# Kernel optimization log

Measured on AMD Instinct MI355X. Metric: run time of the kernel, lower is better.

## Reference

```python
import jax, jax.numpy as jnp
import numpy as np

TEMPERATURE = 0.1


def setup_inputs() -> dict:
    key = jax.random.key(0)
    k1, k2 = jax.random.split(key)
    pred = jax.random.normal(k1, (4, 64, 32), dtype=jnp.float32)
    target = jax.random.normal(k2, (4, 64, 32), dtype=jnp.float32)
    return {"pred": pred, "target": target}


def reference(pred, target):
    # All inputs are finite and no mask is given, so valid_both is all-True and
    # the torch boolean flatten pred[valid_both] is exactly a reshape(-1).
    p = pred.reshape(-1)
    t = target.reshape(-1)
    n = p.shape[0]  # 8192
    # diff[i, j] = x[j] - x[i]; product is symmetric so orientation is irrelevant.
    pd = p[None, :] - p[:, None]           # [n, n]
    td = t[None, :] - t[:, None]           # [n, n]
    agreement = jnp.tanh(pd * td / TEMPERATURE)
    # mean over strict upper triangle (i < j): mask-and-sum, divide by pair count.
    upper = jnp.triu(jnp.ones((n, n), dtype=agreement.dtype), k=1)
    n_pairs = jnp.asarray(n * (n - 1) // 2, dtype=agreement.dtype)
    tau = jnp.sum(agreement * upper) / n_pairs
    return tau
```

## Files before the change

### kernel.cpp

```cpp
#include <hip/hip_runtime.h>


#define NTOT 8192
#define TPB  512
#define KPT  (NTOT / TPB)
#define JBLK 8
#define NBLK (NTOT / JBLK)

__global__ __launch_bounds__(TPB) void ktau_partial(const float* __restrict__ pred,
                                                    const float* __restrict__ targ,
                                                    double* __restrict__ partial) {
    const float C = 28.853900817779268f;
    const int tid = threadIdx.x;
    const int j0  = blockIdx.x * JBLK;

    float pj[JBLK], tj[JBLK];
#pragma unroll
    for (int jj = 0; jj < JBLK; ++jj) {
        pj[jj] = pred[j0 + jj];
        tj[jj] = targ[j0 + jj] * C;
    }

    float pi[KPT], ti[KPT];
#pragma unroll
    for (int k = 0; k < KPT; ++k) {
        const int i = tid + k * TPB;
        pi[k] = pred[i];
        ti[k] = targ[i] * C;
    }

    float acc[JBLK];
#pragma unroll
    for (int jj = 0; jj < JBLK; ++jj) acc[jj] = 0.0f;

#pragma unroll 2
    for (int k = 0; k < KPT; ++k) {
#pragma unroll
        for (int jj = 0; jj < JBLK; ++jj) {
            const float x = (pi[k] - pj[jj]) * (ti[k] - tj[jj]);
            const float e = __builtin_amdgcn_exp2f(x);
            const float r = __builtin_amdgcn_rcpf(e + 1.0f);
            acc[jj] = __builtin_fmaf(-2.0f, r, acc[jj]);
        }
    }

    float fsum = 0.0f;
#pragma unroll
    for (int jj = 0; jj < JBLK; ++jj) fsum += acc[jj];

    double dacc = (double)fsum;
#pragma unroll
    for (int off = 32; off > 0; off >>= 1)
        dacc += __shfl_down(dacc, off, 64);

    __shared__ double red[TPB / 64];
    const int wave = tid >> 6;
    if ((tid & 63) == 0) red[wave] = dacc;
    __syncthreads();
    if (tid == 0) {
        double s = 0.0;
#pragma unroll
        for (int w = 0; w < TPB / 64; ++w) s += red[w];
        partial[blockIdx.x] = s + (double)(TPB * KPT * JBLK);
    }
}

__global__ __launch_bounds__(256) void ktau_final(const double* __restrict__ partial,
                                                  float* __restrict__ out) {
    const int tid = threadIdx.x;
    double s = partial[tid] + partial[tid + 256] + partial[tid + 512] + partial[tid + 768];
#pragma unroll
    for (int off = 32; off > 0; off >>= 1)
        s += __shfl_down(s, off, 64);
    __shared__ double red[4];
    if ((tid & 63) == 0) red[tid >> 6] = s;
    __syncthreads();
    if (tid == 0) {
        const double t = red[0] + red[1] + red[2] + red[3];
        out[0] = (float)(t / ((double)NTOT * (double)(NTOT - 1)));
    }
}

extern "C" void kernel_launch(void* const* d_in, const int* in_sizes, int n_in,
                              void* d_out, int out_size, void* d_ws, size_t ws_size,
                              hipStream_t stream) {
    const float* pred = (const float*)d_in[0];
    const float* targ = (const float*)d_in[1];
    float* out = (float*)d_out;
    double* partial = (double*)d_ws;

    ktau_partial<<<NBLK, TPB, 0, stream>>>(pred, targ, partial);
    ktau_final<<<1, 256, 0, stream>>>(partial, out);
}
```

Baseline: 71.44 us.

## Exploit pair symmetry by computing only upper-triangular tile pairs

Replaces the full n×n sweep with a triangular grid of 128×128 tile pairs, decoding the tile row and column from the block index with a sqrt. Diagonal tiles are halved and the normaliser becomes the pair count, so roughly half of the exp/rcp evaluations are skipped. The j values are staged in shared memory and read as float4, at the cost of a per-block index decode, a barrier, and more partials in the final reduction.

```diff
diff --git a/kernel.cpp b/kernel.cpp
--- a/kernel.cpp
+++ b/kernel.cpp
@@ -2,42 +2,58 @@
 
 
 #define NTOT 8192
-#define TPB  512
-#define KPT  (NTOT / TPB)
-#define JBLK 8
-#define NBLK (NTOT / JBLK)
+#define TILE 128
+#define NT   (NTOT / TILE)
+#define NBLK (NT * (NT + 1) / 2)
+#define TPB  256
 
-__global__ __launch_bounds__(TPB) void ktau_partial(const float* __restrict__ pred,
-                                                    const float* __restrict__ targ,
-                                                    double* __restrict__ partial) {
+__device__ __forceinline__ int rowoff(int a) {
+    return a * NT - (a * (a - 1)) / 2;
+}
+
+__global__ __launch_bounds__(TPB) void ktau_tri(const float* __restrict__ pred,
+                                                const float* __restrict__ targ,
+                                                double* __restrict__ partial) {
     const float C = 28.853900817779268f;
     const int tid = threadIdx.x;
-    const int j0  = blockIdx.x * JBLK;
+    const int bid = blockIdx.x;
 
-    float pj[JBLK], tj[JBLK];
-#pragma unroll
-    for (int jj = 0; jj < JBLK; ++jj) {
-        pj[jj] = pred[j0 + jj];
-        tj[jj] = targ[j0 + jj] * C;
+    int a = (int)((2.0 * NT + 1.0 -
+                   sqrt((2.0 * NT + 1.0) * (2.0 * NT + 1.0) - 8.0 * (double)bid)) * 0.5);
+    while (rowoff(a + 1) <= bid) ++a;
+    while (a > 0 && rowoff(a) > bid) --a;
+    const int b = a + (bid - rowoff(a));
+
+    __shared__ float sjp[TILE];
+    __shared__ float sjt[TILE];
+    if (tid < TILE) {
+        sjp[tid] = pred[b * TILE + tid];
+        sjt[tid] = targ[b * TILE + tid] * C;
     }
 
-    float pi[KPT], ti[KPT];
+    const int il = tid & (TILE - 1);
+    const int jh = tid >> 7;
+    const float pi = pred[a * TILE + il];
+    const float ti = targ[a * TILE + il] * C;
+    __syncthreads();
+
+    float acc[8];
 #pragma unroll
-    for (int k = 0; k < KPT; ++k) {
-        const int i = tid + k * TPB;
-        pi[k] = pred[i];
-        ti[k] = targ[i] * C;
-    }
+    for (int jj = 0; jj < 8; ++jj) acc[jj] = 0.0f;
 
-    float acc[JBLK];
+    const float4* sp4 = (const float4*)sjp;
+    const float4* st4 = (const float4*)sjt;
+
 #pragma unroll
-    for (int jj = 0; jj < JBLK; ++jj) acc[jj] = 0.0f;
-
-#pragma unroll 2
-    for (int k = 0; k < KPT; ++k) {
+    for (int jc = 0; jc < 8; ++jc) {
+        const int q = jh * 16 + jc * 2;
+        const float4 pj0 = sp4[q],     pj1 = sp4[q + 1];
+        const float4 tj0 = st4[q],     tj1 = st4[q + 1];
+        const float pj[8] = {pj0.x, pj0.y, pj0.z, pj0.w, pj1.x, pj1.y, pj1.z, pj1.w};
+        const float tj[8] = {tj0.x, tj0.y, tj0.z, tj0.w, tj1.x, tj1.y, tj1.z, tj1.w};
 #pragma unroll
-        for (int jj = 0; jj < JBLK; ++jj) {
-            const float x = (pi[k] - pj[jj]) * (ti[k] - tj[jj]);
+        for (int jj = 0; jj < 8; ++jj) {
+            const float x = (pi - pj[jj]) * (ti - tj[jj]);
             const float e = __builtin_amdgcn_exp2f(x);
             const float r = __builtin_amdgcn_rcpf(e + 1.0f);
             acc[jj] = __builtin_fmaf(-2.0f, r, acc[jj]);
@@ -46,7 +62,7 @@
 
     float fsum = 0.0f;
 #pragma unroll
-    for (int jj = 0; jj < JBLK; ++jj) fsum += acc[jj];
+    for (int jj = 0; jj < 8; ++jj) fsum += acc[jj];
 
     double dacc = (double)fsum;
 #pragma unroll
@@ -54,21 +70,22 @@
         dacc += __shfl_down(dacc, off, 64);
 
     __shared__ double red[TPB / 64];
-    const int wave = tid >> 6;
-    if ((tid & 63) == 0) red[wave] = dacc;
+    if ((tid & 63) == 0) red[tid >> 6] = dacc;
     __syncthreads();
     if (tid == 0) {
         double s = 0.0;
 #pragma unroll
         for (int w = 0; w < TPB / 64; ++w) s += red[w];
-        partial[blockIdx.x] = s + (double)(TPB * KPT * JBLK);
+        s += (double)(TPB * 64);
+        partial[bid] = (a == b) ? 0.5 * s : s;
     }
 }
 
 __global__ __launch_bounds__(256) void ktau_final(const double* __restrict__ partial,
                                                   float* __restrict__ out) {
     const int tid = threadIdx.x;
-    double s = partial[tid] + partial[tid + 256] + partial[tid + 512] + partial[tid + 768];
+    double s = 0.0;
+    for (int t = tid; t < NBLK; t += 256) s += partial[t];
 #pragma unroll
     for (int off = 32; off > 0; off >>= 1)
         s += __shfl_down(s, off, 64);
@@ -76,8 +93,8 @@
     if ((tid & 63) == 0) red[tid >> 6] = s;
     __syncthreads();
     if (tid == 0) {
-        const double t = red[0] + red[1] + red[2] + red[3];
-        out[0] = (float)(t / ((double)NTOT * (double)(NTOT - 1)));
+        const double n_pairs = (double)NTOT * (double)(NTOT - 1) * 0.5;
+        out[0] = (float)((red[0] + red[1] + red[2] + red[3]) / n_pairs);
     }
 }
 
@@ -89,6 +106,6 @@
     float* out = (float*)d_out;
     double* partial = (double*)d_ws;
 
-    ktau_partial<<<NBLK, TPB, 0, stream>>>(pred, targ, partial);
+    ktau_tri<<<NBLK, TPB, 0, stream>>>(pred, targ, partial);
     ktau_final<<<1, 256, 0, stream>>>(partial, out);
 }
```

Result: faster. 67.06 us (-6.1%).
